# Performance work log

Measured on AMD Instinct MI355X. Metric: run time of the kernel, lower is better.

The kernel has to match this reference:

```python
import jax, jax.numpy as jnp
import numpy as np

B, N, C = 8, 2048, 1024
H = 16                      # num_heads
D = C // H                  # head_dim = 64
SCALE = D ** -0.5
EPS = 1e-5


def _ln(x, gamma, beta):
    mu = jnp.mean(x, axis=-1, keepdims=True)
    var = jnp.mean(jnp.square(x - mu), axis=-1, keepdims=True)
    return (x - mu) * jax.lax.rsqrt(var + EPS) * gamma + beta


def setup_inputs() -> dict:
    key = jax.random.key(0)
    ks = jax.random.split(key, 16)
    s = 0.02
    return {
        "x": jax.random.normal(ks[0], (B, N, C), jnp.float32),
        "context": jax.random.normal(ks[1], (B, N, 2 * C), jnp.float32),
        # shared LayerNorm (self.norm used three times)
        "gamma": jnp.ones((C,), jnp.float32),
        "beta": jnp.zeros((C,), jnp.float32),
        # nn.MultiheadAttention params
        "w_in": jax.random.normal(ks[2], (3 * C, C), jnp.float32) * s,
        "b_in": jnp.zeros((3 * C,), jnp.float32),
        "w_out": jax.random.normal(ks[3], (C, C), jnp.float32) * s,
        "b_out": jnp.zeros((C,), jnp.float32),
        # cross-attn projections
        "wq": jax.random.normal(ks[4], (C, C), jnp.float32) * s,
        "bq": jnp.zeros((C,), jnp.float32),
        "wkv": jax.random.normal(ks[5], (2 * C, 2 * C), jnp.float32) * s,
        "bkv": jnp.zeros((2 * C,), jnp.float32),
        # FFN
        "w1": jax.random.normal(ks[6], (4 * C, C), jnp.float32) * s,
        "b1": jnp.zeros((4 * C,), jnp.float32),
        "w2": jax.random.normal(ks[7], (C, 4 * C), jnp.float32) * s,
        "b2": jnp.zeros((C,), jnp.float32),
    }


def reference(x, context, gamma, beta, w_in, b_in, w_out, b_out,
              wq, bq, wkv, bkv, w1, b1, w2, b2):
    # ---- self-attention (torch MHA, batch_first=False: dim0=B is the SEQ axis) ----
    xn = _ln(x, gamma, beta)
    qkv = xn @ w_in.T + b_in                      # [B, N, 3C]
    q, k, v = jnp.split(qkv, 3, axis=-1)
    q = q.reshape(B, N, H, D)
    k = k.reshape(B, N, H, D)
    v = v.reshape(B, N, H, D)
    # attention over the B axis (i,j index dim0); n is the effective batch
    scores = jnp.einsum('inhd,jnhd->nhij', q, k) * SCALE   # [N, H, B, B]
    attn = jax.nn.softmax(scores, axis=-1)
    sa = jnp.einsum('nhij,jnhd->inhd', attn, v).reshape(B, N, C)
    sa = sa @ w_out.T + b_out
    x = x + sa                                     # dropout = identity (eval)

    # ---- cross-attention (head-summed scores, quirk of the source einsum) ----
    xn = _ln(x, gamma, beta)
    q = (xn @ wq.T + bq).reshape(B, N, H, D).transpose(0, 2, 1, 3)       # [B,H,N,D]
    kv = context @ wkv.T + bkv                     # [B, N, 2C]
    k, v = jnp.split(kv, 2, axis=-1)
    k = k.reshape(B, N, H, D).transpose(0, 2, 1, 3)
    v = v.reshape(B, N, H, D).transpose(0, 2, 1, 3)
    # NOTE: sums over heads h AND d -> single [B,N,N] score map shared by all heads
    scores = jnp.einsum('bhnd,bhmd->bnm', q, k) * SCALE
    attn = jax.nn.softmax(scores, axis=-1)         # [B, N, N]
    out = jnp.einsum('bnm,bhmd->bhnd', attn, v)    # [B, H, N, D]
    out = out.transpose(0, 2, 1, 3).reshape(B, N, C)
    x = out + x

    # ---- FFN ----
    xn = _ln(x, gamma, beta)
    h1 = jax.nn.relu(xn @ w1.T + b1)               # [B, N, 4C]
    x = x + (h1 @ w2.T + b2)
    return x
```

## Files before the change

### kernel.cpp

```cpp
#include <hip/hip_runtime.h>
#include <hip/hip_bf16.h>
#include <stdint.h>

using u16 = unsigned short;
typedef __attribute__((ext_vector_type(8))) short short8;
typedef __attribute__((ext_vector_type(8))) unsigned short ushort8;
typedef __attribute__((ext_vector_type(4))) unsigned short ushort4v;
typedef __attribute__((ext_vector_type(4))) float f32x4;

__device__ __forceinline__ float b2f(u16 b) {
  union { unsigned u; float f; } c; c.u = ((unsigned)b) << 16; return c.f;
}
__device__ __forceinline__ u16 f2b(float f) {
  union { float f; unsigned u; } c; c.f = f;
  unsigned u = c.u;
  return (u16)((u + 0x7FFFu + ((u >> 16) & 1u)) >> 16);
}

__global__ __launch_bounds__(256) void cvt_bf16_kernel(const float* __restrict__ in,
                                                       u16* __restrict__ out, long n) {
  long i = ((long)blockIdx.x * 256 + threadIdx.x) * 8;
  if (i >= n) return;
  float4 a = *(const float4*)(in + i);
  float4 b = *(const float4*)(in + i + 4);
  ushort8 o;
  o[0]=f2b(a.x); o[1]=f2b(a.y); o[2]=f2b(a.z); o[3]=f2b(a.w);
  o[4]=f2b(b.x); o[5]=f2b(b.y); o[6]=f2b(b.z); o[7]=f2b(b.w);
  *(ushort8*)(out + i) = o;
}

__global__ __launch_bounds__(256) void ln_bf16_kernel(const float* __restrict__ x,
    const float* __restrict__ gamma, const float* __restrict__ beta,
    u16* __restrict__ out) {
  size_t row = blockIdx.x;
  int t = threadIdx.x;
  float4 v = ((const float4*)(x + row * 1024))[t];
  float s  = v.x + v.y + v.z + v.w;
  float s2 = v.x*v.x + v.y*v.y + v.z*v.z + v.w*v.w;
  #pragma unroll
  for (int o = 32; o; o >>= 1) { s += __shfl_xor(s, o); s2 += __shfl_xor(s2, o); }
  __shared__ float rs[4], rq[4];
  int w = t >> 6;
  if ((t & 63) == 0) { rs[w] = s; rq[w] = s2; }
  __syncthreads();
  s  = rs[0] + rs[1] + rs[2] + rs[3];
  s2 = rq[0] + rq[1] + rq[2] + rq[3];
  float mu  = s * (1.0f / 1024.0f);
  float var = fmaxf(s2 * (1.0f / 1024.0f) - mu * mu, 0.0f);
  float rr  = rsqrtf(var + 1e-5f);
  float4 g  = ((const float4*)gamma)[t];
  float4 bb = ((const float4*)beta)[t];
  ushort4v o;
  o[0] = f2b((v.x - mu) * rr * g.x + bb.x);
  o[1] = f2b((v.y - mu) * rr * g.y + bb.y);
  o[2] = f2b((v.z - mu) * rr * g.z + bb.z);
  o[3] = f2b((v.w - mu) * rr * g.w + bb.w);
  *(ushort4v*)(out + row * 1024 + t * 4) = o;
}

#define BM 128
#define BN 128
#define BK 64

__device__ __forceinline__ void gload16(const void* g, void* l) {
  __builtin_amdgcn_global_load_lds(
      (const __attribute__((address_space(1))) void*)g,
      (__attribute__((address_space(3))) void*)l, 16, 0, 0);
}

template<int HAS_BIAS, int RELU, int HAS_RES, int OUT_BF16>
__global__ __launch_bounds__(256)
void gemm_bt(const u16* __restrict__ A, const u16* __restrict__ W,
             const float* __restrict__ bias, const float* __restrict__ res,
             void* __restrict__ Cv,
             int M, int Nn, int K, int lda, int ldb, int ldc,
             long long sAz, long long sWz, long long sCz, long long sRz,
             float scale)
{
  A += (size_t)blockIdx.z * sAz;
  W += (size_t)blockIdx.z * sWz;
  if (HAS_RES) res += (size_t)blockIdx.z * sRz;
  const size_t cz = (size_t)blockIdx.z * sCz;

  const int tid = threadIdx.x;
  const int i0 = blockIdx.y * BM;
  const int j0 = blockIdx.x * BN;
  __shared__ u16 sA[BM][BK];
  __shared__ u16 sB[BN][BK];
  const int lane = tid & 63;
  const int wv = tid >> 6, wr = wv >> 1, wc = wv & 1;
  const int r16 = lane & 15, kg = lane >> 4;
  const int crow = tid >> 3;
  const int ccol = (tid & 7) * 8;

  f32x4 acc[4][4] = {};

  for (int k0 = 0; k0 < K; k0 += BK) {
    #pragma unroll
    for (int p = 0; p < 4; ++p) {
      int row = p * 32 + crow;
      gload16(A + (size_t)(i0 + row) * lda + k0 + ccol, &sA[row][ccol]);
    }
    #pragma unroll
    for (int p = 0; p < 4; ++p) {
      int row = p * 32 + crow;
      gload16(W + (size_t)(j0 + row) * ldb + k0 + ccol, &sB[row][ccol]);
    }
    __syncthreads();
    #pragma unroll
    for (int kk = 0; kk < 2; ++kk) {
      short8 a[4], b[4];
      #pragma unroll
      for (int i = 0; i < 4; ++i)
        a[i] = *(const short8*)&sA[wr * 64 + i * 16 + r16][kk * 32 + kg * 8];
      #pragma unroll
      for (int j = 0; j < 4; ++j)
        b[j] = *(const short8*)&sB[wc * 64 + j * 16 + r16][kk * 32 + kg * 8];
      #pragma unroll
      for (int i = 0; i < 4; ++i)
        #pragma unroll
        for (int j = 0; j < 4; ++j)
          acc[i][j] = __builtin_amdgcn_mfma_f32_16x16x32_bf16(a[i], b[j], acc[i][j], 0, 0, 0);
    }
    __syncthreads();
  }

  #pragma unroll
  for (int j = 0; j < 4; ++j) {
    int col = j0 + wc * 64 + j * 16 + r16;
    float bj = HAS_BIAS ? bias[col] : 0.0f;
    #pragma unroll
    for (int i = 0; i < 4; ++i) {
      int row = i0 + wr * 64 + i * 16 + kg * 4;
      #pragma unroll
      for (int r = 0; r < 4; ++r) {
        float v = acc[i][j][r] * scale + bj;
        if (RELU) v = fmaxf(v, 0.0f);
        size_t idx = cz + (size_t)(row + r) * ldc + col;
        if (HAS_RES) v += res[(size_t)(row + r) * ldc + col];
        if (OUT_BF16) ((u16*)Cv)[idx] = f2b(v);
        else          ((float*)Cv)[idx] = v;
      }
    }
  }
}

__global__ __launch_bounds__(256) void self_attn_kernel(const u16* __restrict__ qkv,
                                                        u16* __restrict__ sa) {
  int w = threadIdx.x >> 6, lane = threadIdx.x & 63;
  int unit = blockIdx.x * 4 + w;
  int n = unit >> 4, h = unit & 15;
  __shared__ u16 sQ[4][8][64], sK[4][8][64], sV[4][8][64];
  __shared__ float sP[4][8][8];
  int li = lane >> 3, ld0 = (lane & 7) * 8;
  size_t base = ((size_t)li * 2048 + n) * 3072 + h * 64 + ld0;
  *(ushort8*)&sQ[w][li][ld0] = *(const ushort8*)(qkv + base);
  *(ushort8*)&sK[w][li][ld0] = *(const ushort8*)(qkv + base + 1024);
  *(ushort8*)&sV[w][li][ld0] = *(const ushort8*)(qkv + base + 2048);
  __syncthreads();
  int sj = lane & 7;
  float s = 0.0f;
  #pragma unroll
  for (int c8 = 0; c8 < 8; ++c8) {
    ushort8 q8 = *(const ushort8*)&sQ[w][li][c8 * 8];
    ushort8 k8 = *(const ushort8*)&sK[w][sj][c8 * 8];
    #pragma unroll
    for (int q = 0; q < 8; ++q) s += b2f(q8[q]) * b2f(k8[q]);
  }
  s *= 0.125f;
  float m = fmaxf(s, __shfl_xor(s, 1));
  m = fmaxf(m, __shfl_xor(m, 2));
  m = fmaxf(m, __shfl_xor(m, 4));
  float e = __expf(s - m);
  float sum = e;
  sum += __shfl_xor(sum, 1); sum += __shfl_xor(sum, 2); sum += __shfl_xor(sum, 4);
  sP[w][li][sj] = e / sum;
  __syncthreads();
  float o[8] = {0,0,0,0,0,0,0,0};
  #pragma unroll
  for (int j = 0; j < 8; ++j) {
    float pj = sP[w][li][j];
    ushort8 v8 = *(const ushort8*)&sV[w][j][ld0];
    #pragma unroll
    for (int dd = 0; dd < 8; ++dd) o[dd] += pj * b2f(v8[dd]);
  }
  ushort8 ov;
  #pragma unroll
  for (int dd = 0; dd < 8; ++dd) ov[dd] = f2b(o[dd]);
  *(ushort8*)(sa + ((size_t)li * 2048 + n) * 1024 + h * 64 + ld0) = ov;
}

__global__ __launch_bounds__(256) void softmax_kernel(const float* __restrict__ s,
                                                      u16* __restrict__ p) {
  size_t row = blockIdx.x;
  const float4* sr = (const float4*)(s + row * 2048);
  int t = threadIdx.x;
  float4 a = sr[t * 2], b = sr[t * 2 + 1];
  float e[8] = {a.x, a.y, a.z, a.w, b.x, b.y, b.z, b.w};
  float mx = e[0];
  #pragma unroll
  for (int q = 1; q < 8; ++q) mx = fmaxf(mx, e[q]);
  #pragma unroll
  for (int o = 32; o; o >>= 1) mx = fmaxf(mx, __shfl_xor(mx, o));
  __shared__ float rm[4], rsum[4];
  int w = t >> 6;
  if ((t & 63) == 0) rm[w] = mx;
  __syncthreads();
  mx = fmaxf(fmaxf(rm[0], rm[1]), fmaxf(rm[2], rm[3]));
  float sum = 0.0f;
  #pragma unroll
  for (int q = 0; q < 8; ++q) { e[q] = __expf(e[q] - mx); sum += e[q]; }
  #pragma unroll
  for (int o = 32; o; o >>= 1) sum += __shfl_xor(sum, o);
  if ((t & 63) == 0) rsum[w] = sum;
  __syncthreads();
  sum = rsum[0] + rsum[1] + rsum[2] + rsum[3];
  float inv = 1.0f / sum;
  ushort8 o8;
  #pragma unroll
  for (int q = 0; q < 8; ++q) o8[q] = f2b(e[q] * inv);
  *(ushort8*)(p + row * 2048 + t * 8) = o8;
}

__global__ __launch_bounds__(256) void transpose_v_kernel(const u16* __restrict__ kv,
                                                          u16* __restrict__ vT) {
  __shared__ u16 tile[64][72];
  int b = blockIdx.z;
  int m0 = blockIdx.x * 64, c0 = blockIdx.y * 64;
  int t = threadIdx.x;
  int r = t >> 2, cc = (t & 3) * 16;
  const u16* src = kv + ((size_t)b * 2048 + m0 + r) * 2048 + 1024 + c0 + cc;
  *(ushort8*)&tile[r][cc]     = *(const ushort8*)src;
  *(ushort8*)&tile[r][cc + 8] = *(const ushort8*)(src + 8);
  __syncthreads();
  int rc = t >> 2, mm0 = (t & 3) * 16;
  ushort8 o1, o2;
  #pragma unroll
  for (int q = 0; q < 8; ++q) { o1[q] = tile[mm0 + q][rc]; o2[q] = tile[mm0 + 8 + q][rc]; }
  u16* dst = vT + ((size_t)b * 1024 + c0 + rc) * 2048 + m0 + mm0;
  *(ushort8*)dst = o1;
  *(ushort8*)(dst + 8) = o2;
}

extern "C" void kernel_launch(void* const* d_in, const int* in_sizes, int n_in,
                              void* d_out, int out_size, void* d_ws, size_t ws_size,
                              hipStream_t stream) {
  const float* x     = (const float*)d_in[0];
  const float* ctx   = (const float*)d_in[1];
  const float* gamma = (const float*)d_in[2];
  const float* beta  = (const float*)d_in[3];
  const float* w_in  = (const float*)d_in[4];
  const float* b_in  = (const float*)d_in[5];
  const float* w_out = (const float*)d_in[6];
  const float* b_out = (const float*)d_in[7];
  const float* wq    = (const float*)d_in[8];
  const float* bq    = (const float*)d_in[9];
  const float* wkv   = (const float*)d_in[10];
  const float* bkv   = (const float*)d_in[11];
  const float* w1    = (const float*)d_in[12];
  const float* b1    = (const float*)d_in[13];
  const float* w2    = (const float*)d_in[14];
  const float* b2    = (const float*)d_in[15];
  float* xout = (float*)d_out;

  char* p = (char*)d_ws;
  auto take = [&](size_t bytes) { char* r = p; p += (bytes + 255) & ~(size_t)255; return r; };
  u16* wbi  = (u16*)take((size_t)3145728 * 2);
  u16* wbo  = (u16*)take((size_t)1048576 * 2);
  u16* wbq  = (u16*)take((size_t)1048576 * 2);
  u16* wbkv = (u16*)take((size_t)4194304 * 2);
  u16* wb1  = (u16*)take((size_t)4194304 * 2);
  u16* wb2  = (u16*)take((size_t)4194304 * 2);
  u16* xnb  = (u16*)take((size_t)16777216 * 2);
  u16* sab  = (u16*)take((size_t)16777216 * 2);
  float* x1 = (float*)take((size_t)16777216 * 4);
  u16* kvb  = (u16*)take((size_t)33554432 * 2);
  u16* ctxb = (u16*)take((size_t)33554432 * 2);
  char* big = take((size_t)134217728);
  u16*   qkvb    = (u16*)big;
  float* scoresf = (float*)big;
  u16*   h1b     = (u16*)big;
  u16*   probs   = ctxb;
  u16*   qb      = sab;
  u16*   vTb     = sab;

  dim3 blk(256);
  auto cvt = [&](const float* in, u16* out, long n) {
    cvt_bf16_kernel<<<dim3((unsigned)(n / 2048)), blk, 0, stream>>>(in, out, n);
  };
  cvt(w_in,  wbi,  3145728);
  cvt(w_out, wbo,  1048576);
  cvt(wq,    wbq,  1048576);
  cvt(wkv,   wbkv, 4194304);
  cvt(w1,    wb1,  4194304);
  cvt(w2,    wb2,  4194304);
  cvt(ctx,   ctxb, 33554432);

  ln_bf16_kernel<<<dim3(16384), blk, 0, stream>>>(x, gamma, beta, xnb);
  gemm_bt<1,0,0,1><<<dim3(24, 128, 1), blk, 0, stream>>>(xnb, wbi, b_in, nullptr, qkvb,
      16384, 3072, 1024, 1024, 1024, 3072, 0, 0, 0, 0, 1.0f);
  self_attn_kernel<<<dim3(8192), blk, 0, stream>>>(qkvb, sab);
  gemm_bt<1,0,1,0><<<dim3(8, 128, 1), blk, 0, stream>>>(sab, wbo, b_out, x, x1,
      16384, 1024, 1024, 1024, 1024, 1024, 0, 0, 0, 0, 1.0f);

  ln_bf16_kernel<<<dim3(16384), blk, 0, stream>>>(x1, gamma, beta, xnb);
  gemm_bt<1,0,0,1><<<dim3(8, 128, 1), blk, 0, stream>>>(xnb, wbq, bq, nullptr, qb,
      16384, 1024, 1024, 1024, 1024, 1024, 0, 0, 0, 0, 1.0f);
  gemm_bt<1,0,0,1><<<dim3(16, 128, 1), blk, 0, stream>>>(ctxb, wbkv, bkv, nullptr, kvb,
      16384, 2048, 2048, 2048, 2048, 2048, 0, 0, 0, 0, 1.0f);
  gemm_bt<0,0,0,0><<<dim3(16, 16, 8), blk, 0, stream>>>(qb, kvb, nullptr, nullptr, scoresf,
      2048, 2048, 1024, 1024, 2048, 2048,
      2048LL * 1024, 2048LL * 2048, 2048LL * 2048, 0, 0.125f);
  softmax_kernel<<<dim3(16384), blk, 0, stream>>>(scoresf, probs);
  transpose_v_kernel<<<dim3(32, 16, 8), blk, 0, stream>>>(kvb, vTb);
  gemm_bt<0,0,1,0><<<dim3(8, 16, 8), blk, 0, stream>>>(probs, vTb, nullptr, x1, xout,
      2048, 1024, 2048, 2048, 2048, 1024,
      2048LL * 2048, 1024LL * 2048, 2048LL * 1024, 2048LL * 1024, 1.0f);

  ln_bf16_kernel<<<dim3(16384), blk, 0, stream>>>(xout, gamma, beta, xnb);
  gemm_bt<1,1,0,1><<<dim3(32, 128, 1), blk, 0, stream>>>(xnb, wb1, b1, nullptr, h1b,
      16384, 4096, 1024, 1024, 1024, 4096, 0, 0, 0, 0, 1.0f);
  gemm_bt<1,0,1,0><<<dim3(8, 128, 1), blk, 0, stream>>>(h1b, wb2, b2, xout, xout,
      16384, 1024, 4096, 4096, 4096, 1024, 0, 0, 0, 0, 1.0f);
}
```

Baseline: 1.637 ms.

## Double-buffer GEMM LDS tiles and remap workgroups across XCDs

The GEMM main loop now uses two LDS buffers, so the global-to-LDS loads for the next K tile are issued while MFMAs run on the current tile, hiding memory latency behind compute. Workgroup ids are also remapped so consecutive logical tiles land on the same XCD, which is meant to improve L2 reuse of A/W tiles on the multi-die MI355X. The cost is double the LDS per block, which may reduce occupancy, and the remap assumes round-robin XCD dispatch of 8.

```diff
diff --git a/kernel.cpp b/kernel.cpp
--- a/kernel.cpp
+++ b/kernel.cpp
@@ -82,11 +82,19 @@
   if (HAS_RES) res += (size_t)blockIdx.z * sRz;
   const size_t cz = (size_t)blockIdx.z * sCz;
 
+  const int gx = gridDim.x;
+  const int nwg = gx * gridDim.y;
+  const int orig = blockIdx.y * gx + blockIdx.x;
+  const int q = nwg >> 3, r = nwg & 7;
+  const int xcd = orig & 7;
+  const int cbase = (xcd < r) ? xcd * (q + 1) : r * (q + 1) + (xcd - r) * q;
+  const int logical = cbase + (orig >> 3);
+  const int i0 = (logical / gx) * BM;
+  const int j0 = (logical % gx) * BN;
+
   const int tid = threadIdx.x;
-  const int i0 = blockIdx.y * BM;
-  const int j0 = blockIdx.x * BN;
-  __shared__ u16 sA[BM][BK];
-  __shared__ u16 sB[BN][BK];
+  __shared__ u16 sA[2][BM][BK];
+  __shared__ u16 sB[2][BN][BK];
   const int lane = tid & 63;
   const int wv = tid >> 6, wr = wv >> 1, wc = wv & 1;
   const int r16 = lane & 15, kg = lane >> 4;
@@ -95,27 +103,33 @@
 
   f32x4 acc[4][4] = {};
 
-  for (int k0 = 0; k0 < K; k0 += BK) {
+  auto stage = [&](int c, int k0) {
     #pragma unroll
     for (int p = 0; p < 4; ++p) {
       int row = p * 32 + crow;
-      gload16(A + (size_t)(i0 + row) * lda + k0 + ccol, &sA[row][ccol]);
+      gload16(A + (size_t)(i0 + row) * lda + k0 + ccol, &sA[c][row][ccol]);
     }
     #pragma unroll
     for (int p = 0; p < 4; ++p) {
       int row = p * 32 + crow;
-      gload16(W + (size_t)(j0 + row) * ldb + k0 + ccol, &sB[row][ccol]);
+      gload16(W + (size_t)(j0 + row) * ldb + k0 + ccol, &sB[c][row][ccol]);
     }
-    __syncthreads();
+  };
+
+  stage(0, 0);
+  __syncthreads();
+  int c = 0;
+  for (int k0 = 0; k0 < K; k0 += BK) {
+    if (k0 + BK < K) stage(c ^ 1, k0 + BK);
     #pragma unroll
     for (int kk = 0; kk < 2; ++kk) {
       short8 a[4], b[4];
       #pragma unroll
       for (int i = 0; i < 4; ++i)
-        a[i] = *(const short8*)&sA[wr * 64 + i * 16 + r16][kk * 32 + kg * 8];
+        a[i] = *(const short8*)&sA[c][wr * 64 + i * 16 + r16][kk * 32 + kg * 8];
       #pragma unroll
       for (int j = 0; j < 4; ++j)
-        b[j] = *(const short8*)&sB[wc * 64 + j * 16 + r16][kk * 32 + kg * 8];
+        b[j] = *(const short8*)&sB[c][wc * 64 + j * 16 + r16][kk * 32 + kg * 8];
       #pragma unroll
       for (int i = 0; i < 4; ++i)
         #pragma unroll
@@ -123,6 +137,7 @@
           acc[i][j] = __builtin_amdgcn_mfma_f32_16x16x32_bf16(a[i], b[j], acc[i][j], 0, 0, 0);
     }
     __syncthreads();
+    c ^= 1;
   }
 
   #pragma unroll
@@ -133,11 +148,11 @@
     for (int i = 0; i < 4; ++i) {
       int row = i0 + wr * 64 + i * 16 + kg * 4;
       #pragma unroll
-      for (int r = 0; r < 4; ++r) {
-        float v = acc[i][j][r] * scale + bj;
+      for (int r2 = 0; r2 < 4; ++r2) {
+        float v = acc[i][j][r2] * scale + bj;
         if (RELU) v = fmaxf(v, 0.0f);
-        size_t idx = cz + (size_t)(row + r) * ldc + col;
-        if (HAS_RES) v += res[(size_t)(row + r) * ldc + col];
+        size_t idx = cz + (size_t)(row + r2) * ldc + col;
+        if (HAS_RES) v += res[(size_t)(row + r2) * ldc + col];
         if (OUT_BF16) ((u16*)Cv)[idx] = f2b(v);
         else          ((float*)Cv)[idx] = v;
       }
```

Result: no change. 1.630 ms (-0.4%).
